# Optimization experiments

Measured on AMD Instinct MI355X. Metric: run time of the kernel, lower is better.

The kernel has to match this reference:

```python
import jax, jax.numpy as jnp
import numpy as np

E = 1024
H = 16
F = 4096
B, S = 4, 2048
LN_EPS = 1e-5


def setup_inputs() -> dict:
    key = jax.random.key(0)
    ks = jax.random.split(key, 12)
    sE = 1.0 / np.sqrt(E)
    sF = 1.0 / np.sqrt(F)
    return {
        "x": jax.random.normal(ks[0], (B, S, E), dtype=jnp.float32),
        # attention projections (torch Linear weight layout [out,in], bias=False)
        "Wq": jax.random.uniform(ks[1], (E, E), jnp.float32, -sE, sE),
        "Wk": jax.random.uniform(ks[2], (E, E), jnp.float32, -sE, sE),
        "Wv": jax.random.uniform(ks[3], (E, E), jnp.float32, -sE, sE),
        "Wo": jax.random.uniform(ks[4], (E, E), jnp.float32, -sE, sE),
        # LayerNorms
        "g1": jnp.ones((E,), jnp.float32),
        "b1": jnp.zeros((E,), jnp.float32),
        "g2": jnp.ones((E,), jnp.float32),
        "b2": jnp.zeros((E,), jnp.float32),
        # FFN (classical): linear1 [F,E], linear2 [E,F]
        "W1": jax.random.uniform(ks[5], (F, E), jnp.float32, -sE, sE),
        "bb1": jax.random.uniform(ks[6], (F,), jnp.float32, -sE, sE),
        "W2": jax.random.uniform(ks[7], (E, F), jnp.float32, -sF, sF),
        "bb2": jax.random.uniform(ks[8], (F,), jnp.float32, -sF, sF)[:E] * 0 + jax.random.uniform(ks[9], (E,), jnp.float32, -sF, sF),
    }


def _layernorm(x, g, b):
    mu = jnp.mean(x, axis=-1, keepdims=True)
    var = jnp.mean(jnp.square(x - mu), axis=-1, keepdims=True)
    return (x - mu) * jax.lax.rsqrt(var + LN_EPS) * g + b


def reference(x, Wq, Wk, Wv, Wo, g1, b1, g2, b2, W1, bb1, W2, bb2):
    b, s, _ = x.shape
    hd = E // H
    # projections: torch Linear is x @ W.T
    q = (x @ Wq.T).reshape(b, s, H, hd).transpose(0, 2, 1, 3)  # [B,H,S,hd]
    k = (x @ Wk.T).reshape(b, s, H, hd).transpose(0, 2, 1, 3)
    v = (x @ Wv.T).reshape(b, s, H, hd).transpose(0, 2, 1, 3)
    scores = jnp.einsum('bhqd,bhkd->bhqk', q, k) / jnp.sqrt(jnp.float32(hd))
    probs = jax.nn.softmax(scores, axis=-1)
    attn = jnp.einsum('bhqk,bhkd->bhqd', probs, v)
    attn = attn.transpose(0, 2, 1, 3).reshape(b, s, E)
    attn_out = attn @ Wo.T
    # residual + LN (dropout=0 / eval)
    h = _layernorm(x + attn_out, g1, b1)
    # FFN
    ffn = jax.nn.relu(h @ W1.T + bb1) @ W2.T + bb2
    return _layernorm(h + ffn, g2, b2)
```

## Files before the change

kernel.cpp:

```cpp
#include <hip/hip_runtime.h>
#include <stdint.h>

#define E_DIM   1024
#define H_NUM   16
#define HD      64
#define F_DIM   4096
#define B_NUM   4
#define S_LEN   2048
#define M_ROWS  (B_NUM * S_LEN)
#define QKV_LD  3072

typedef unsigned short u16;
typedef __bf16 bf16_t;
typedef bf16_t  bf16x8 __attribute__((ext_vector_type(8)));
typedef u16     u16x8  __attribute__((ext_vector_type(8)));
typedef float   f32x4  __attribute__((ext_vector_type(4)));
typedef float   f32x16 __attribute__((ext_vector_type(16)));
typedef unsigned u32x4 __attribute__((ext_vector_type(4)));

#define AS1 __attribute__((address_space(1)))
#define AS3 __attribute__((address_space(3)))

__device__ __forceinline__ void gload_lds16(const void* g, void* l) {
    __builtin_amdgcn_global_load_lds((AS1 void*)g, (AS3 void*)l, 16, 0, 0);
}

__device__ __forceinline__ u16 f2b(float f) {
    union { float f; unsigned u; } a; a.f = f;
    unsigned u = a.u + 0x7fffu + ((a.u >> 16) & 1u);
    return (u16)(u >> 16);
}
__device__ __forceinline__ float b2f(u16 v) {
    union { unsigned u; float f; } a; a.u = ((unsigned)v) << 16;
    return a.f;
}

__device__ __forceinline__ unsigned cvt_pk_bf16(float lo, float hi) {
    unsigned r;
    asm("v_cvt_pk_bf16_f32 %0, %1, %2" : "=v"(r) : "v"(lo), "v"(hi));
    return r;
}

__device__ __forceinline__ int swz_c(int row) {
    return ((row & 7) << 4) ^ ((row & 8) << 2);
}
__device__ __forceinline__ int swz8(int row) {
    return (row & 7) << 4;
}

#define VM_WAIT(n) asm volatile("s_waitcnt vmcnt(" #n ")" ::: "memory")
#define SC_LOG2E 0.1803368801111204f

struct CastArgs {
    const float* src[7];
    u16* dst[7];
    float scale[7];
    unsigned cum4[8];
};

__global__ __launch_bounds__(256) void cast_multi(CastArgs a) {
    const int total = a.cum4[7];
    const int stride = gridDim.x * blockDim.x;
    for (int i = blockIdx.x * blockDim.x + threadIdx.x; i < total; i += stride) {
        int s = 0;
#pragma unroll
        for (int k = 1; k < 7; ++k) s += (i >= (int)a.cum4[k]);
        const int off = i - (int)a.cum4[s];
        const float sc = a.scale[s];
        float4 v = reinterpret_cast<const float4*>(a.src[s])[off];
        ushort4 o;
        o.x = f2b(v.x * sc); o.y = f2b(v.y * sc); o.z = f2b(v.z * sc); o.w = f2b(v.w * sc);
        reinterpret_cast<ushort4*>(a.dst[s])[off] = o;
    }
}

__device__ __forceinline__ void store_c(float* C, size_t idx, float v) { C[idx] = v; }
__device__ __forceinline__ void store_c(u16* C, size_t idx, float v)   { C[idx] = f2b(v); }

template <typename OutT, bool RELU, bool HASBIAS, int K, bool VSPLIT>
__global__ __launch_bounds__(256, 2)
void gemm2n(const u16* __restrict__ A, const u16* __restrict__ B,
            OutT* __restrict__ C, const float* __restrict__ bias,
            char* __restrict__ VtG, int M, int N) {
    constexpr int NT = K / 32;
    __shared__ __align__(16) char smem[3 * 24576];

    const int tid  = threadIdx.x;
    const int lane = tid & 63, wave = tid >> 6;
    const int lr   = lane & 15, kh = lane >> 4;
    const int wr   = wave >> 1, wc = wave & 1;

    const int nwg = gridDim.x * gridDim.y;
    int wg = blockIdx.y * gridDim.x + blockIdx.x;
    const int cpx = nwg >> 3;
    wg = (wg & 7) * cpx + (wg >> 3);
    const int bx = wg % gridDim.x, by = wg / gridDim.x;
    const int row0 = by * 256, col0 = bx * 128;

    const int srow = tid >> 2, scolb = (tid & 3) * 16;
    const char* Ag = (const char*)(A + (size_t)(row0 + srow) * K) + scolb;
    const char* Bg = (const char*)(B + (size_t)(col0 + srow) * K) + scolb;
    const size_t rstep = (size_t)64 * K * 2;

    auto stage = [&](int t) {
        char* s = smem + (t % 3) * 24576;
        const size_t ko = (size_t)t * 64;
#pragma unroll
        for (int r = 0; r < 4; ++r)
            gload_lds16(Ag + r * rstep + ko, s + r * 4096 + tid * 16);
#pragma unroll
        for (int r = 0; r < 2; ++r)
            gload_lds16(Bg + r * rstep + ko, s + 16384 + r * 4096 + tid * 16);
    };

    f32x4 acc[8][4] = {};
    stage(0); stage(1);

    for (int t = 0; t < NT; ++t) {
        if (t + 1 < NT) VM_WAIT(6);
        else            VM_WAIT(0);
        __builtin_amdgcn_s_barrier();
        __builtin_amdgcn_sched_barrier(0);
        if (t + 2 < NT) stage(t + 2);

        const char* s = smem + (t % 3) * 24576;
        bf16x8 af[8], bf[4];
#pragma unroll
        for (int m = 0; m < 8; ++m)
            af[m] = *(const bf16x8*)(s + (wr * 128 + m * 16 + lr) * 64 + kh * 16);
#pragma unroll
        for (int n = 0; n < 4; ++n)
            bf[n] = *(const bf16x8*)(s + 16384 + (wc * 64 + n * 16 + lr) * 64 + kh * 16);

        __builtin_amdgcn_s_setprio(1);
#pragma unroll
        for (int m = 0; m < 8; ++m)
#pragma unroll
            for (int n = 0; n < 4; ++n)
                acc[m][n] = __builtin_amdgcn_mfma_f32_16x16x32_bf16(af[m], bf[n], acc[m][n], 0, 0, 0);
        __builtin_amdgcn_s_setprio(0);
    }

    if (VSPLIT && col0 >= 2048) {
#pragma unroll
        for (int m = 0; m < 8; ++m) {
#pragma unroll
            for (int n = 0; n < 4; ++n) {
                const int colv = col0 - 2048 + wc * 64 + n * 16 + lr;
                const int h = colv >> 6, d = colv & 63;
                const int rowq = row0 + wr * 128 + m * 16 + kh * 4;
                const int bq = rowq >> 11, sq = rowq & 2047;
                const int kvt = sq >> 6, kl = sq & 63;
                const int g = kl >> 4, qb = kl & 12;
                const int slotq = ((qb & 4) << 1) | ((qb & 8) >> 1) | (qb & 3);
                const size_t byte_off = ((size_t)((bq * H_NUM + h) * HD + d) << 12)
                                        + kvt * 128 + ((((g << 4) + slotq) << 1) ^ swz8(d));
                const u16 p0 = f2b(acc[m][n][0]), p1 = f2b(acc[m][n][1]);
                const u16 p2 = f2b(acc[m][n][2]), p3 = f2b(acc[m][n][3]);
                uint2 pk;
                pk.x = (unsigned)p0 | ((unsigned)p1 << 16);
                pk.y = (unsigned)p2 | ((unsigned)p3 << 16);
                *(uint2*)(VtG + byte_off) = pk;
            }
        }
        return;
    }

#pragma unroll
    for (int m = 0; m < 8; ++m) {
#pragma unroll
        for (int n = 0; n < 4; ++n) {
            int col = col0 + wc * 64 + n * 16 + lr;
            float bv = 0.f;
            if constexpr (HASBIAS) bv = bias[col];
#pragma unroll
            for (int r = 0; r < 4; ++r) {
                int row = row0 + wr * 128 + m * 16 + kh * 4 + r;
                float v = acc[m][n][r] + bv;
                if constexpr (RELU) v = fmaxf(v, 0.f);
                store_c(C, (size_t)row * N + col, v);
            }
        }
    }
}

template <typename OutT, bool RELU, bool HASBIAS, int K>
__global__ __launch_bounds__(256, 3)
void gemm2h(const u16* __restrict__ A, const u16* __restrict__ B,
            OutT* __restrict__ C, const float* __restrict__ bias,
            int M, int N) {
    constexpr int NT = K / 32;
    __shared__ __align__(16) char smem[3 * 16384];

    const int tid  = threadIdx.x;
    const int lane = tid & 63, wave = tid >> 6;
    const int lr   = lane & 15, kh = lane >> 4;
    const int wr   = wave >> 1, wc = wave & 1;

    const int nwg = gridDim.x * gridDim.y;
    int wg = blockIdx.y * gridDim.x + blockIdx.x;
    const int cpx = nwg >> 3;
    wg = (wg & 7) * cpx + (wg >> 3);
    const int bx = wg % gridDim.x, by = wg / gridDim.x;
    const int row0 = by * 128, col0 = bx * 128;

    const int srow = tid >> 2;
    const int scolb = (tid & 3) * 16;
    const char* Ag = (const char*)(A + (size_t)(row0 + srow) * K) + scolb;
    const char* Bg = (const char*)(B + (size_t)(col0 + srow) * K) + scolb;
    const size_t rstep = (size_t)64 * K * 2;

    auto do_stage = [&](int t) {
        char* s = smem + (t % 3) * 16384;
        const size_t ko = (size_t)t * 64;
        gload_lds16(Ag + ko,         s + tid * 16);
        gload_lds16(Ag + rstep + ko, s + 4096 + tid * 16);
        gload_lds16(Bg + ko,         s + 8192 + tid * 16);
        gload_lds16(Bg + rstep + ko, s + 12288 + tid * 16);
    };

    f32x4 acc[4][4] = {};
    do_stage(0); do_stage(1);

    for (int t = 0; t < NT; ++t) {
        if (t + 1 < NT) VM_WAIT(4);
        else            VM_WAIT(0);
        __builtin_amdgcn_s_barrier();
        __builtin_amdgcn_sched_barrier(0);
        if (t + 2 < NT) do_stage(t + 2);

        const char* s = smem + (t % 3) * 16384;
        bf16x8 af[4], bf[4];
#pragma unroll
        for (int m = 0; m < 4; ++m)
            af[m] = *(const bf16x8*)(s + (wr * 64 + m * 16 + lr) * 64 + kh * 16);
#pragma unroll
        for (int n = 0; n < 4; ++n)
            bf[n] = *(const bf16x8*)(s + 8192 + (wc * 64 + n * 16 + lr) * 64 + kh * 16);

        __builtin_amdgcn_s_setprio(1);
#pragma unroll
        for (int m = 0; m < 4; ++m)
#pragma unroll
            for (int n = 0; n < 4; ++n)
                acc[m][n] = __builtin_amdgcn_mfma_f32_16x16x32_bf16(af[m], bf[n], acc[m][n], 0, 0, 0);
        __builtin_amdgcn_s_setprio(0);
    }

#pragma unroll
    for (int m = 0; m < 4; ++m) {
#pragma unroll
        for (int n = 0; n < 4; ++n) {
            int col = col0 + wc * 64 + n * 16 + lr;
            float bv = 0.f;
            if constexpr (HASBIAS) bv = bias[col];
#pragma unroll
            for (int r = 0; r < 4; ++r) {
                int row = row0 + wr * 64 + m * 16 + kh * 4 + r;
                float v = acc[m][n][r] + bv;
                if constexpr (RELU) v = fmaxf(v, 0.f);
                store_c(C, (size_t)row * N + col, v);
            }
        }
    }
}

__global__ __launch_bounds__(512, 4)
void attn_kernel(const u16* __restrict__ QKV, const char* __restrict__ VtG,
                 u16* __restrict__ Ob) {
    __shared__ char Ks[2][64 * 128];
    __shared__ char Vt[2][64 * 128];

    const int tid  = threadIdx.x;
    const int lane = tid & 63, wave = tid >> 6;
    const int l31  = lane & 31, hi = lane >> 5;
    const int bid  = blockIdx.x;
    const int bh   = bid & 63;
    const int q0   = (bid >> 6) * 256;
    const int h    = bh & 15;
    const int b    = bh >> 4;

    const u16* Q  = QKV;
    const u16* Kp = QKV + 1024;

    const size_t qrow = (size_t)(b * S_LEN + q0 + wave * 32 + l31);
    bf16x8 qf[4];
#pragma unroll
    for (int c = 0; c < 4; ++c)
        qf[c] = *(const bf16x8*)(Q + qrow * QKV_LD + h * HD + c * 16 + hi * 8);

    bf16x8 ones;
#pragma unroll
    for (int j = 0; j < 8; ++j) ones[j] = (bf16_t)1.0f;

    f32x16 o0 = {}, o1 = {}, accl = {};

    const char* Kg  = (const char*)(Kp + (size_t)(b * S_LEN) * QKV_LD + h * HD);
    const char* Vgb = VtG + ((size_t)((b * H_NUM + h) * HD) << 12);

    const int ob      = wave * 1024 + lane * 16;
    const int st_row  = ob >> 7;
    const int st_colb = ob & 127;
    const int kst_colb = st_colb ^ swz_c(st_row);
    const int st_lds  = wave * 1024;
    const int krd = l31 * 128;
    const int vrd = l31 * 128;

    gload_lds16(Kg + (size_t)st_row * (QKV_LD * 2) + kst_colb, Ks[0] + st_lds);
    gload_lds16(Vgb + (size_t)st_row * 4096 + st_colb,         Vt[0] + st_lds);
    __syncthreads();

    const int NT = S_LEN / 64;
    for (int t = 0; t < NT; ++t) {
        const int cur = t & 1;
        if (t < NT - 1) {
            const int kv0n = (t + 1) * 64;
            gload_lds16(Kg + (size_t)(kv0n + st_row) * (QKV_LD * 2) + kst_colb,
                        Ks[cur ^ 1] + st_lds);
            gload_lds16(Vgb + (size_t)st_row * 4096 + (t + 1) * 128 + st_colb,
                        Vt[cur ^ 1] + st_lds);
        }

#pragma unroll
        for (int half = 0; half < 2; ++half) {
            const char* ksb = Ks[cur] + half * 4096 + krd;
            f32x16 st = {};
#pragma unroll
            for (int c = 0; c < 4; ++c) {
                bf16x8 kf = *(const bf16x8*)(ksb + ((c * 32 + hi * 16) ^ swz_c(l31)));
                st = __builtin_amdgcn_mfma_f32_32x32x16_bf16(kf, qf[c], st, 0, 0, 0);
            }

#pragma unroll
            for (int i = 0; i < 16; ++i)
                st[i] = __builtin_amdgcn_exp2f(st[i]);

            unsigned w[8];
#pragma unroll
            for (int i = 0; i < 8; ++i) w[i] = cvt_pk_bf16(st[2 * i], st[2 * i + 1]);

#pragma unroll
            for (int cc = 0; cc < 2; ++cc) {
                u32x4 fw;
                fw[0] = w[4 * cc];     fw[1] = w[4 * cc + 1];
                fw[2] = w[4 * cc + 2]; fw[3] = w[4 * cc + 3];
                bf16x8 pf = __builtin_bit_cast(bf16x8, fw);
                const int colb = (half * 64 + cc * 32 + hi * 16) ^ swz8(l31);
                bf16x8 v0 = *(const bf16x8*)(Vt[cur] + vrd + colb);
                bf16x8 v1 = *(const bf16x8*)(Vt[cur] + 4096 + vrd + colb);
                o0   = __builtin_amdgcn_mfma_f32_32x32x16_bf16(v0, pf, o0, 0, 0, 0);
                o1   = __builtin_amdgcn_mfma_f32_32x32x16_bf16(v1, pf, o1, 0, 0, 0);
                accl = __builtin_amdgcn_mfma_f32_32x32x16_bf16(ones, pf, accl, 0, 0, 0);
            }
        }
        __syncthreads();
    }

    const float inv = 1.0f / accl[0];
    unsigned m0[16], xx[16];
#pragma unroll
    for (int g = 0; g < 4; ++g)
#pragma unroll
        for (int u = 0; u < 2; ++u) {
            int r = g * 4 + 2 * u;
            m0[2 * g + u]     = cvt_pk_bf16(o0[r] * inv, o0[r + 1] * inv);
            m0[8 + 2 * g + u] = cvt_pk_bf16(o1[r] * inv, o1[r + 1] * inv);
        }
#pragma unroll
    for (int i = 0; i < 16; ++i) xx[i] = __shfl_xor(m0[i], 32);

    {
        unsigned full[8], sec[8];
#pragma unroll
        for (int g = 0; g < 4; ++g) {
            full[2 * g + 0] = hi ? xx[8 + 2 * g]     : m0[2 * g];
            full[2 * g + 1] = hi ? xx[8 + 2 * g + 1] : m0[2 * g + 1];
            sec[2 * g + 0]  = hi ? m0[8 + 2 * g]     : xx[2 * g];
            sec[2 * g + 1]  = hi ? m0[8 + 2 * g + 1] : xx[2 * g + 1];
        }
        u32x4 out0, out1, out2, out3;
        out0[0] = full[0]; out0[1] = full[1]; out0[2] = sec[0]; out0[3] = sec[1];
        out1[0] = full[2]; out1[1] = full[3]; out1[2] = sec[2]; out1[3] = sec[3];
        out2[0] = full[4]; out2[1] = full[5]; out2[2] = sec[4]; out2[3] = sec[5];
        out3[0] = full[6]; out3[1] = full[7]; out3[2] = sec[6]; out3[3] = sec[7];
        u16* op = Ob + qrow * E_DIM + h * HD + hi * 32;
        *(u32x4*)(op)      = out0;
        *(u32x4*)(op + 8)  = out1;
        *(u32x4*)(op + 16) = out2;
        *(u32x4*)(op + 24) = out3;
    }
}

template <typename XA>
__device__ __forceinline__ float4 ld4(const XA* p, size_t idx) {
    if constexpr (sizeof(XA) == 2) {
        ushort4 v = reinterpret_cast<const ushort4*>(p)[idx];
        float4 o; o.x = b2f(v.x); o.y = b2f(v.y); o.z = b2f(v.z); o.w = b2f(v.w);
        return o;
    } else {
        return reinterpret_cast<const float4*>(p)[idx];
    }
}

template <typename XA, typename XB>
__global__ __launch_bounds__(256)
void add_ln(const XA* __restrict__ xa, const XB* __restrict__ xb2,
            const float* __restrict__ g, const float* __restrict__ be,
            float* __restrict__ of, u16* __restrict__ ob) {
    const int row = blockIdx.x;
    const int t = threadIdx.x;
    const int lane = t & 63, wave = t >> 6;

    float4 va = ld4<XA>(xa + (size_t)row * E_DIM, t);
    float4 vb = ld4<XB>(xb2 + (size_t)row * E_DIM, t);
    float v0 = va.x + vb.x, v1 = va.y + vb.y, v2 = va.z + vb.z, v3 = va.w + vb.w;
    float s  = v0 + v1 + v2 + v3;
    float s2 = v0 * v0 + v1 * v1 + v2 * v2 + v3 * v3;
#pragma unroll
    for (int m = 32; m >= 1; m >>= 1) {
        s  += __shfl_xor(s, m);
        s2 += __shfl_xor(s2, m);
    }
    __shared__ float red[8];
    if (lane == 0) { red[wave] = s; red[4 + wave] = s2; }
    __syncthreads();
    s  = red[0] + red[1] + red[2] + red[3];
    s2 = red[4] + red[5] + red[6] + red[7];

    float mu   = s * (1.0f / E_DIM);
    float var  = s2 * (1.0f / E_DIM) - mu * mu;
    float rstd = rsqrtf(var + 1e-5f);

    float4 gg = reinterpret_cast<const float4*>(g)[t];
    float4 bb = reinterpret_cast<const float4*>(be)[t];
    float y0 = (v0 - mu) * rstd * gg.x + bb.x;
    float y1 = (v1 - mu) * rstd * gg.y + bb.y;
    float y2 = (v2 - mu) * rstd * gg.z + bb.z;
    float y3 = (v3 - mu) * rstd * gg.w + bb.w;
    if (of) {
        float4 o; o.x = y0; o.y = y1; o.z = y2; o.w = y3;
        reinterpret_cast<float4*>(of + (size_t)row * E_DIM)[t] = o;
    }
    if (ob) {
        ushort4 o;
        o.x = f2b(y0); o.y = f2b(y1); o.z = f2b(y2); o.w = f2b(y3);
        reinterpret_cast<ushort4*>(ob + (size_t)row * E_DIM)[t] = o;
    }
}

extern "C" void kernel_launch(void* const* d_in, const int* in_sizes, int n_in,
                              void* d_out, int out_size, void* d_ws, size_t ws_size,
                              hipStream_t stream) {
    const float* x   = (const float*)d_in[0];
    const float* Wq  = (const float*)d_in[1];
    const float* Wk  = (const float*)d_in[2];
    const float* Wv  = (const float*)d_in[3];
    const float* Wo  = (const float*)d_in[4];
    const float* g1  = (const float*)d_in[5];
    const float* b1  = (const float*)d_in[6];
    const float* g2  = (const float*)d_in[7];
    const float* b2  = (const float*)d_in[8];
    const float* W1  = (const float*)d_in[9];
    const float* bb1 = (const float*)d_in[10];
    const float* W2  = (const float*)d_in[11];
    const float* bb2 = (const float*)d_in[12];
    float* out = (float*)d_out;

    char* ws = (char*)d_ws;
    const size_t MB = 1024ull * 1024ull;
    u16* wqkvb = (u16*)(ws + 0 * MB);
    u16* wob   = (u16*)(ws + 6 * MB);
    u16* w1b   = (u16*)(ws + 8 * MB);
    u16* w2b   = (u16*)(ws + 16 * MB);
    u16* xb    = (u16*)(ws + 24 * MB);
    u16* qkvb  = (u16*)(ws + 40 * MB);
    u16* attnb = (u16*)(ws + 88 * MB);
    u16* attno = (u16*)(ws + 104 * MB);
    u16* hb    = (u16*)(ws + 136 * MB);
    char* VtG  = (ws + 152 * MB);
    u16* ffn1  = (u16*)(ws + 24 * MB);
    u16* y2b   = (u16*)(ws + 104 * MB);

    dim3 blk(256);

    CastArgs ca;
    ca.src[0] = x;   ca.dst[0] = xb;                            ca.scale[0] = 1.f;
    ca.src[1] = Wq;  ca.dst[1] = wqkvb;                         ca.scale[1] = SC_LOG2E;
    ca.src[2] = Wk;  ca.dst[2] = wqkvb + E_DIM * E_DIM;         ca.scale[2] = 1.f;
    ca.src[3] = Wv;  ca.dst[3] = wqkvb + 2 * E_DIM * E_DIM;     ca.scale[3] = 1.f;
    ca.src[4] = Wo;  ca.dst[4] = wob;                           ca.scale[4] = 1.f;
    ca.src[5] = W1;  ca.dst[5] = w1b;                           ca.scale[5] = 1.f;
    ca.src[6] = W2;  ca.dst[6] = w2b;                           ca.scale[6] = 1.f;
    unsigned n4[7] = {M_ROWS * E_DIM / 4, E_DIM * E_DIM / 4, E_DIM * E_DIM / 4,
                      E_DIM * E_DIM / 4, E_DIM * E_DIM / 4, F_DIM * E_DIM / 4,
                      E_DIM * F_DIM / 4};
    ca.cum4[0] = 0;
    for (int i = 0; i < 7; ++i) ca.cum4[i + 1] = ca.cum4[i] + n4[i];
    cast_multi<<<dim3(2048), blk, 0, stream>>>(ca);

    gemm2n<u16, false, false, E_DIM, true><<<dim3(QKV_LD / 128, M_ROWS / 256), blk, 0, stream>>>(
        xb, wqkvb, qkvb, nullptr, VtG, M_ROWS, QKV_LD);

    attn_kernel<<<dim3(512), dim3(512), 0, stream>>>(qkvb, VtG, attnb);

    gemm2h<u16, false, false, E_DIM><<<dim3(E_DIM / 128, M_ROWS / 128), blk, 0, stream>>>(
        attnb, wob, attno, nullptr, M_ROWS, E_DIM);

    add_ln<u16, u16><<<dim3(M_ROWS), blk, 0, stream>>>(xb, attno, g1, b1, nullptr, hb);

    gemm2n<u16, true, true, E_DIM, false><<<dim3(F_DIM / 128, M_ROWS / 256), blk, 0, stream>>>(
        hb, w1b, ffn1, bb1, nullptr, M_ROWS, F_DIM);

    gemm2h<u16, false, true, F_DIM><<<dim3(E_DIM / 128, M_ROWS / 128), blk, 0, stream>>>(
        ffn1, w2b, y2b, bb2, M_ROWS, E_DIM);

    add_ln<u16, u16><<<dim3(M_ROWS), blk, 0, stream>>>(hb, y2b, g2, b2, out, nullptr);
}
```

Baseline: 350.0 us.

## Split-K the FFN down-projection and fold partial sums into final LayerNorm

Replaces the 128x128-tile FFN2 GEMM over K=4096 with the 256x128-tile gemm2n kernel split into two K halves along grid z. Each half writes bf16 partials to separate buffers, and a new add_ln_sk kernel sums both partials, the residual and the bias before the final LayerNorm. This is meant to raise the number of workgroups and use the larger-tile kernel for the long-K GEMM. In exchange it adds extra partial-buffer traffic and rounds each partial to bf16, which costs some precision.

New measurement: 346.3 us. Within noise of the previous version (-1.0%).

```diff
diff --git a/kernel.cpp b/kernel.cpp
--- a/kernel.cpp
+++ b/kernel.cpp
@@ -77,12 +77,12 @@
 __device__ __forceinline__ void store_c(float* C, size_t idx, float v) { C[idx] = v; }
 __device__ __forceinline__ void store_c(u16* C, size_t idx, float v)   { C[idx] = f2b(v); }
 
-template <typename OutT, bool RELU, bool HASBIAS, int K, bool VSPLIT>
+template <typename OutT, bool RELU, bool HASBIAS, int K, int KSPAN, bool VSPLIT>
 __global__ __launch_bounds__(256, 2)
 void gemm2n(const u16* __restrict__ A, const u16* __restrict__ B,
             OutT* __restrict__ C, const float* __restrict__ bias,
             char* __restrict__ VtG, int M, int N) {
-    constexpr int NT = K / 32;
+    constexpr int NT = KSPAN / 32;
     __shared__ __align__(16) char smem[3 * 24576];
 
     const int tid  = threadIdx.x;
@@ -96,11 +96,13 @@
     wg = (wg & 7) * cpx + (wg >> 3);
     const int bx = wg % gridDim.x, by = wg / gridDim.x;
     const int row0 = by * 256, col0 = bx * 128;
+    const int koff = blockIdx.z * KSPAN;
 
     const int srow = tid >> 2, scolb = (tid & 3) * 16;
-    const char* Ag = (const char*)(A + (size_t)(row0 + srow) * K) + scolb;
-    const char* Bg = (const char*)(B + (size_t)(col0 + srow) * K) + scolb;
+    const char* Ag = (const char*)(A + (size_t)(row0 + srow) * K + koff) + scolb;
+    const char* Bg = (const char*)(B + (size_t)(col0 + srow) * K + koff) + scolb;
     const size_t rstep = (size_t)64 * K * 2;
+    OutT* Cz = C + (size_t)blockIdx.z * M * N;
 
     auto stage = [&](int t) {
         char* s = smem + (t % 3) * 24576;
@@ -178,7 +180,7 @@
                 int row = row0 + wr * 128 + m * 16 + kh * 4 + r;
                 float v = acc[m][n][r] + bv;
                 if constexpr (RELU) v = fmaxf(v, 0.f);
-                store_c(C, (size_t)row * N + col, v);
+                store_c(Cz, (size_t)row * N + col, v);
             }
         }
     }
@@ -446,6 +448,50 @@
         o.x = f2b(y0); o.y = f2b(y1); o.z = f2b(y2); o.w = f2b(y3);
         reinterpret_cast<ushort4*>(ob + (size_t)row * E_DIM)[t] = o;
     }
+}
+
+__global__ __launch_bounds__(256)
+void add_ln_sk(const u16* __restrict__ xa, const u16* __restrict__ p0,
+               const u16* __restrict__ p1, const float* __restrict__ bias,
+               const float* __restrict__ g, const float* __restrict__ be,
+               float* __restrict__ of) {
+    const int row = blockIdx.x;
+    const int t = threadIdx.x;
+    const int lane = t & 63, wave = t >> 6;
+
+    float4 va = ld4<u16>(xa + (size_t)row * E_DIM, t);
+    float4 vp0 = ld4<u16>(p0 + (size_t)row * E_DIM, t);
+    float4 vp1 = ld4<u16>(p1 + (size_t)row * E_DIM, t);
+    float4 bi = reinterpret_cast<const float4*>(bias)[t];
+    float v0 = va.x + vp0.x + vp1.x + bi.x;
+    float v1 = va.y + vp0.y + vp1.y + bi.y;
+    float v2 = va.z + vp0.z + vp1.z + bi.z;
+    float v3 = va.w + vp0.w + vp1.w + bi.w;
+    float s  = v0 + v1 + v2 + v3;
+    float s2 = v0 * v0 + v1 * v1 + v2 * v2 + v3 * v3;
+#pragma unroll
+    for (int m = 32; m >= 1; m >>= 1) {
+        s  += __shfl_xor(s, m);
+        s2 += __shfl_xor(s2, m);
+    }
+    __shared__ float red[8];
+    if (lane == 0) { red[wave] = s; red[4 + wave] = s2; }
+    __syncthreads();
+    s  = red[0] + red[1] + red[2] + red[3];
+    s2 = red[4] + red[5] + red[6] + red[7];
+
+    float mu   = s * (1.0f / E_DIM);
+    float var  = s2 * (1.0f / E_DIM) - mu * mu;
+    float rstd = rsqrtf(var + 1e-5f);
+
+    float4 gg = reinterpret_cast<const float4*>(g)[t];
+    float4 bb = reinterpret_cast<const float4*>(be)[t];
+    float4 o;
+    o.x = (v0 - mu) * rstd * gg.x + bb.x;
+    o.y = (v1 - mu) * rstd * gg.y + bb.y;
+    o.z = (v2 - mu) * rstd * gg.z + bb.z;
+    o.w = (v3 - mu) * rstd * gg.w + bb.w;
+    reinterpret_cast<float4*>(of + (size_t)row * E_DIM)[t] = o;
 }
 
 extern "C" void kernel_launch(void* const* d_in, const int* in_sizes, int n_in,
@@ -479,7 +525,7 @@
     u16* hb    = (u16*)(ws + 136 * MB);
     char* VtG  = (ws + 152 * MB);
     u16* ffn1  = (u16*)(ws + 24 * MB);
-    u16* y2b   = (u16*)(ws + 104 * MB);
+    u16* psk   = (u16*)(ws + 104 * MB);
 
     dim3 blk(256);
 
@@ -498,7 +544,7 @@
     for (int i = 0; i < 7; ++i) ca.cum4[i + 1] = ca.cum4[i] + n4[i];
     cast_multi<<<dim3(2048), blk, 0, stream>>>(ca);
 
-    gemm2n<u16, false, false, E_DIM, true><<<dim3(QKV_LD / 128, M_ROWS / 256), blk, 0, stream>>>(
+    gemm2n<u16, false, false, E_DIM, E_DIM, true><<<dim3(QKV_LD / 128, M_ROWS / 256), blk, 0, stream>>>(
         xb, wqkvb, qkvb, nullptr, VtG, M_ROWS, QKV_LD);
 
     attn_kernel<<<dim3(512), dim3(512), 0, stream>>>(qkvb, VtG, attnb);
@@ -508,11 +554,12 @@
 
     add_ln<u16, u16><<<dim3(M_ROWS), blk, 0, stream>>>(xb, attno, g1, b1, nullptr, hb);
 
-    gemm2n<u16, true, true, E_DIM, false><<<dim3(F_DIM / 128, M_ROWS / 256), blk, 0, stream>>>(
+    gemm2n<u16, true, true, E_DIM, E_DIM, false><<<dim3(F_DIM / 128, M_ROWS / 256), blk, 0, stream>>>(
         hb, w1b, ffn1, bb1, nullptr, M_ROWS, F_DIM);
 
-    gemm2h<u16, false, true, F_DIM><<<dim3(E_DIM / 128, M_ROWS / 128), blk, 0, stream>>>(
-        ffn1, w2b, y2b, bb2, M_ROWS, E_DIM);
-
-    add_ln<u16, u16><<<dim3(M_ROWS), blk, 0, stream>>>(hb, y2b, g2, b2, out, nullptr);
-}
+    gemm2n<u16, false, false, F_DIM, F_DIM / 2, false><<<dim3(E_DIM / 128, M_ROWS / 256, 2), blk, 0, stream>>>(
+        ffn1, w2b, psk, nullptr, nullptr, M_ROWS, E_DIM);
+
+    add_ln_sk<<<dim3(M_ROWS), blk, 0, stream>>>(
+        hb, psk, psk + (size_t)M_ROWS * E_DIM, bb2, g2, b2, out);
+}
```

## Split-K the N=1024 GEMMs with 256-row tiles and reduce partials inside LayerNorm

Applied to the files above, without the earlier changes.

Removes the 128x128 gemm2h kernel. The two N=1024 GEMMs (output projection and FFN down-projection) now use the 256x128 gemm2n tile with a 2-way split-K over grid z, writing two bf16 partials. A new add_ln_sk kernel sums the residual, both partials and the optional bias before LayerNorm. Separately, the attention row-sum MFMA is issued once per half on pre-summed probabilities instead of once per 32-column chunk. This targets low tile reuse and grid under-fill on the narrow GEMMs, and reduces MFMA count in attention. It costs extra partial-buffer traffic and a second bf16 rounding of the partials, which changes numerics slightly.

New measurement: 349.3 us. Within noise of the previous version (-0.2%).

```diff
diff --git a/kernel.cpp b/kernel.cpp
--- a/kernel.cpp
+++ b/kernel.cpp
@@ -77,12 +77,12 @@
 __device__ __forceinline__ void store_c(float* C, size_t idx, float v) { C[idx] = v; }
 __device__ __forceinline__ void store_c(u16* C, size_t idx, float v)   { C[idx] = f2b(v); }
 
-template <typename OutT, bool RELU, bool HASBIAS, int K, bool VSPLIT>
+template <typename OutT, bool RELU, bool HASBIAS, int K, int KSPAN, bool VSPLIT>
 __global__ __launch_bounds__(256, 2)
 void gemm2n(const u16* __restrict__ A, const u16* __restrict__ B,
             OutT* __restrict__ C, const float* __restrict__ bias,
             char* __restrict__ VtG, int M, int N) {
-    constexpr int NT = K / 32;
+    constexpr int NT = KSPAN / 32;
     __shared__ __align__(16) char smem[3 * 24576];
 
     const int tid  = threadIdx.x;
@@ -96,11 +96,13 @@
     wg = (wg & 7) * cpx + (wg >> 3);
     const int bx = wg % gridDim.x, by = wg / gridDim.x;
     const int row0 = by * 256, col0 = bx * 128;
+    const int koff = blockIdx.z * KSPAN;
 
     const int srow = tid >> 2, scolb = (tid & 3) * 16;
-    const char* Ag = (const char*)(A + (size_t)(row0 + srow) * K) + scolb;
-    const char* Bg = (const char*)(B + (size_t)(col0 + srow) * K) + scolb;
+    const char* Ag = (const char*)(A + (size_t)(row0 + srow) * K + koff) + scolb;
+    const char* Bg = (const char*)(B + (size_t)(col0 + srow) * K + koff) + scolb;
     const size_t rstep = (size_t)64 * K * 2;
+    OutT* Cz = C + (size_t)blockIdx.z * M * N;
 
     auto stage = [&](int t) {
         char* s = smem + (t % 3) * 24576;
@@ -178,88 +180,7 @@
                 int row = row0 + wr * 128 + m * 16 + kh * 4 + r;
                 float v = acc[m][n][r] + bv;
                 if constexpr (RELU) v = fmaxf(v, 0.f);
-                store_c(C, (size_t)row * N + col, v);
-            }
-        }
-    }
-}
-
-template <typename OutT, bool RELU, bool HASBIAS, int K>
-__global__ __launch_bounds__(256, 3)
-void gemm2h(const u16* __restrict__ A, const u16* __restrict__ B,
-            OutT* __restrict__ C, const float* __restrict__ bias,
-            int M, int N) {
-    constexpr int NT = K / 32;
-    __shared__ __align__(16) char smem[3 * 16384];
-
-    const int tid  = threadIdx.x;
-    const int lane = tid & 63, wave = tid >> 6;
-    const int lr   = lane & 15, kh = lane >> 4;
-    const int wr   = wave >> 1, wc = wave & 1;
-
-    const int nwg = gridDim.x * gridDim.y;
-    int wg = blockIdx.y * gridDim.x + blockIdx.x;
-    const int cpx = nwg >> 3;
-    wg = (wg & 7) * cpx + (wg >> 3);
-    const int bx = wg % gridDim.x, by = wg / gridDim.x;
-    const int row0 = by * 128, col0 = bx * 128;
-
-    const int srow = tid >> 2;
-    const int scolb = (tid & 3) * 16;
-    const char* Ag = (const char*)(A + (size_t)(row0 + srow) * K) + scolb;
-    const char* Bg = (const char*)(B + (size_t)(col0 + srow) * K) + scolb;
-    const size_t rstep = (size_t)64 * K * 2;
-
-    auto do_stage = [&](int t) {
-        char* s = smem + (t % 3) * 16384;
-        const size_t ko = (size_t)t * 64;
-        gload_lds16(Ag + ko,         s + tid * 16);
-        gload_lds16(Ag + rstep + ko, s + 4096 + tid * 16);
-        gload_lds16(Bg + ko,         s + 8192 + tid * 16);
-        gload_lds16(Bg + rstep + ko, s + 12288 + tid * 16);
-    };
-
-    f32x4 acc[4][4] = {};
-    do_stage(0); do_stage(1);
-
-    for (int t = 0; t < NT; ++t) {
-        if (t + 1 < NT) VM_WAIT(4);
-        else            VM_WAIT(0);
-        __builtin_amdgcn_s_barrier();
-        __builtin_amdgcn_sched_barrier(0);
-        if (t + 2 < NT) do_stage(t + 2);
-
-        const char* s = smem + (t % 3) * 16384;
-        bf16x8 af[4], bf[4];
-#pragma unroll
-        for (int m = 0; m < 4; ++m)
-            af[m] = *(const bf16x8*)(s + (wr * 64 + m * 16 + lr) * 64 + kh * 16);
-#pragma unroll
-        for (int n = 0; n < 4; ++n)
-            bf[n] = *(const bf16x8*)(s + 8192 + (wc * 64 + n * 16 + lr) * 64 + kh * 16);
-
-        __builtin_amdgcn_s_setprio(1);
-#pragma unroll
-        for (int m = 0; m < 4; ++m)
-#pragma unroll
-            for (int n = 0; n < 4; ++n)
-                acc[m][n] = __builtin_amdgcn_mfma_f32_16x16x32_bf16(af[m], bf[n], acc[m][n], 0, 0, 0);
-        __builtin_amdgcn_s_setprio(0);
-    }
-
-#pragma unroll
-    for (int m = 0; m < 4; ++m) {
-#pragma unroll
-        for (int n = 0; n < 4; ++n) {
-            int col = col0 + wc * 64 + n * 16 + lr;
-            float bv = 0.f;
-            if constexpr (HASBIAS) bv = bias[col];
-#pragma unroll
-            for (int r = 0; r < 4; ++r) {
-                int row = row0 + wr * 64 + m * 16 + kh * 4 + r;
-                float v = acc[m][n][r] + bv;
-                if constexpr (RELU) v = fmaxf(v, 0.f);
-                store_c(C, (size_t)row * N + col, v);
+                store_c(Cz, (size_t)row * N + col, v);
             }
         }
     }
@@ -339,6 +260,13 @@
 #pragma unroll
             for (int i = 0; i < 8; ++i) w[i] = cvt_pk_bf16(st[2 * i], st[2 * i + 1]);
 
+            u32x4 fs;
+#pragma unroll
+            for (int i = 0; i < 4; ++i)
+                fs[i] = cvt_pk_bf16(st[2 * i] + st[2 * i + 8], st[2 * i + 1] + st[2 * i + 9]);
+            bf16x8 pfs = __builtin_bit_cast(bf16x8, fs);
+            accl = __builtin_amdgcn_mfma_f32_32x32x16_bf16(ones, pfs, accl, 0, 0, 0);
+
 #pragma unroll
             for (int cc = 0; cc < 2; ++cc) {
                 u32x4 fw;
@@ -348,9 +276,8 @@
                 const int colb = (half * 64 + cc * 32 + hi * 16) ^ swz8(l31);
                 bf16x8 v0 = *(const bf16x8*)(Vt[cur] + vrd + colb);
                 bf16x8 v1 = *(const bf16x8*)(Vt[cur] + 4096 + vrd + colb);
-                o0   = __builtin_amdgcn_mfma_f32_32x32x16_bf16(v0, pf, o0, 0, 0, 0);
-                o1   = __builtin_amdgcn_mfma_f32_32x32x16_bf16(v1, pf, o1, 0, 0, 0);
-                accl = __builtin_amdgcn_mfma_f32_32x32x16_bf16(ones, pf, accl, 0, 0, 0);
+                o0 = __builtin_amdgcn_mfma_f32_32x32x16_bf16(v0, pf, o0, 0, 0, 0);
+                o1 = __builtin_amdgcn_mfma_f32_32x32x16_bf16(v1, pf, o1, 0, 0, 0);
             }
         }
         __syncthreads();
@@ -402,18 +329,27 @@
     }
 }
 
-template <typename XA, typename XB>
+template <bool HASB>
 __global__ __launch_bounds__(256)
-void add_ln(const XA* __restrict__ xa, const XB* __restrict__ xb2,
-            const float* __restrict__ g, const float* __restrict__ be,
-            float* __restrict__ of, u16* __restrict__ ob) {
+void add_ln_sk(const u16* __restrict__ xa, const u16* __restrict__ p0,
+               const u16* __restrict__ p1, const float* __restrict__ bias,
+               const float* __restrict__ g, const float* __restrict__ be,
+               float* __restrict__ of, u16* __restrict__ ob) {
     const int row = blockIdx.x;
     const int t = threadIdx.x;
     const int lane = t & 63, wave = t >> 6;
 
-    float4 va = ld4<XA>(xa + (size_t)row * E_DIM, t);
-    float4 vb = ld4<XB>(xb2 + (size_t)row * E_DIM, t);
-    float v0 = va.x + vb.x, v1 = va.y + vb.y, v2 = va.z + vb.z, v3 = va.w + vb.w;
+    float4 va  = ld4<u16>(xa + (size_t)row * E_DIM, t);
+    float4 vp0 = ld4<u16>(p0 + (size_t)row * E_DIM, t);
+    float4 vp1 = ld4<u16>(p1 + (size_t)row * E_DIM, t);
+    float v0 = va.x + vp0.x + vp1.x;
+    float v1 = va.y + vp0.y + vp1.y;
+    float v2 = va.z + vp0.z + vp1.z;
+    float v3 = va.w + vp0.w + vp1.w;
+    if constexpr (HASB) {
+        float4 bi = reinterpret_cast<const float4*>(bias)[t];
+        v0 += bi.x; v1 += bi.y; v2 += bi.z; v3 += bi.w;
+    }
     float s  = v0 + v1 + v2 + v3;
     float s2 = v0 * v0 + v1 * v1 + v2 * v2 + v3 * v3;
 #pragma unroll
@@ -475,11 +411,10 @@
     u16* xb    = (u16*)(ws + 24 * MB);
     u16* qkvb  = (u16*)(ws + 40 * MB);
     u16* attnb = (u16*)(ws + 88 * MB);
-    u16* attno = (u16*)(ws + 104 * MB);
     u16* hb    = (u16*)(ws + 136 * MB);
     char* VtG  = (ws + 152 * MB);
     u16* ffn1  = (u16*)(ws + 24 * MB);
-    u16* y2b   = (u16*)(ws + 104 * MB);
+    u16* psk   = (u16*)(ws + 104 * MB);
 
     dim3 blk(256);
 
@@ -498,21 +433,23 @@
     for (int i = 0; i < 7; ++i) ca.cum4[i + 1] = ca.cum4[i] + n4[i];
     cast_multi<<<dim3(2048), blk, 0, stream>>>(ca);
 
-    gemm2n<u16, false, false, E_DIM, true><<<dim3(QKV_LD / 128, M_ROWS / 256), blk, 0, stream>>>(
+    gemm2n<u16, false, false, E_DIM, E_DIM, true><<<dim3(QKV_LD / 128, M_ROWS / 256), blk, 0, stream>>>(
         xb, wqkvb, qkvb, nullptr, VtG, M_ROWS, QKV_LD);
 
     attn_kernel<<<dim3(512), dim3(512), 0, stream>>>(qkvb, VtG, attnb);
 
-    gemm2h<u16, false, false, E_DIM><<<dim3(E_DIM / 128, M_ROWS / 128), blk, 0, stream>>>(
-        attnb, wob, attno, nullptr, M_ROWS, E_DIM);
-
-    add_ln<u16, u16><<<dim3(M_ROWS), blk, 0, stream>>>(xb, attno, g1, b1, nullptr, hb);
-
-    gemm2n<u16, true, true, E_DIM, false><<<dim3(F_DIM / 128, M_ROWS / 256), blk, 0, stream>>>(
+    gemm2n<u16, false, false, E_DIM, E_DIM / 2, false><<<dim3(E_DIM / 128, M_ROWS / 256, 2), blk, 0, stream>>>(
+        attnb, wob, psk, nullptr, nullptr, M_ROWS, E_DIM);
+
+    add_ln_sk<false><<<dim3(M_ROWS), blk, 0, stream>>>(
+        xb, psk, psk + (size_t)M_ROWS * E_DIM, nullptr, g1, b1, nullptr, hb);
+
+    gemm2n<u16, true, true, E_DIM, E_DIM, false><<<dim3(F_DIM / 128, M_ROWS / 256), blk, 0, stream>>>(
         hb, w1b, ffn1, bb1, nullptr, M_ROWS, F_DIM);
 
-    gemm2h<u16, false, true, F_DIM><<<dim3(E_DIM / 128, M_ROWS / 128), blk, 0, stream>>>(
-        ffn1, w2b, y2b, bb2, M_ROWS, E_DIM);
-
-    add_ln<u16, u16><<<dim3(M_ROWS), blk, 0, stream>>>(hb, y2b, g2, b2, out, nullptr);
-}
+    gemm2n<u16, false, false, F_DIM, F_DIM / 2, false><<<dim3(E_DIM / 128, M_ROWS / 256, 2), blk, 0, stream>>>(
+        ffn1, w2b, psk, nullptr, nullptr, M_ROWS, E_DIM);
+
+    add_ln_sk<true><<<dim3(M_ROWS), blk, 0, stream>>>(
+        hb, psk, psk + (size_t)M_ROWS * E_DIM, bb2, g2, b2, out, nullptr);
+}
```
